# Optimization experiments

Hardware: AMD Instinct MI355X
Metric: run time of the kernel (lower is better)

The kernel has to match this reference:

```python
import jax, jax.numpy as jnp
import numpy as np

# Upper-triangular index pattern used by convert_Avec_to_A (row-major triu of 4x4 -> 10 entries)
_TRIU_R, _TRIU_C = np.triu_indices(4)


def _A_vec_to_A(A_vec):
    """(B,10) -> (B,4,4) symmetric matrix, filling upper triangle row-major then mirroring."""
    B = A_vec.shape[0]
    A = jnp.zeros((B, 4, 4), dtype=A_vec.dtype)
    A = A.at[:, _TRIU_R, _TRIU_C].set(A_vec)
    A = A.at[:, _TRIU_C, _TRIU_R].set(A_vec)
    return A


def setup_inputs() -> dict:
    key = jax.random.key(0)
    k1, k2 = jax.random.split(key)
    B = 1048576
    A_vec_pred = jax.random.normal(k1, (B, 10), dtype=jnp.float32)
    q_target = jax.random.normal(k2, (B, 4), dtype=jnp.float32)
    q_target = q_target / jnp.linalg.norm(q_target, axis=-1, keepdims=True)  # unit quaternions
    return {"A_vec_pred": A_vec_pred, "q_target": q_target}


def reference(A_vec_pred, q_target):
    # A_vec_to_quat(-A_vec_pred): eigenvector of minimum eigenvalue of sym(-A_vec)
    A = _A_vec_to_A(-A_vec_pred)                 # (B,4,4)
    _, evs = jnp.linalg.eigh(A)                  # eigenvalues ascending; columns = eigenvectors
    q_pred = evs[:, :, 0]                        # (B,4) min-eigenvalue eigenvector (unit norm)
    # quat_chordal_squared_loss: d = min(||q-qt||, ||q+qt||); losses = 2*d^2*(4-d^2)
    d2 = jnp.minimum(jnp.sum((q_pred - q_target) ** 2, axis=-1),
                     jnp.sum((q_pred + q_target) ** 2, axis=-1))
    losses = 2.0 * d2 * (4.0 - d2)
    return losses.mean()
```

## Files before the change

### kernel.cpp

```cpp
#include <hip/hip_runtime.h>


#define TPB 256
#define PAIRS 2

typedef float vf4 __attribute__((ext_vector_type(4)));

struct Pair { vf4 f0, f1, f2, f3, f4, q0, q1; };

__device__ __forceinline__ void issue_loads(const float* a, const float* q,
                                            Pair& d) {
    unsigned long long aa = (unsigned long long)a;
    unsigned long long qq = (unsigned long long)q;
    asm volatile("global_load_dwordx4 %0, %1, off"           : "=v"(d.f0) : "v"(aa));
    asm volatile("global_load_dwordx4 %0, %1, off offset:16" : "=v"(d.f1) : "v"(aa));
    asm volatile("global_load_dwordx4 %0, %1, off offset:32" : "=v"(d.f2) : "v"(aa));
    asm volatile("global_load_dwordx4 %0, %1, off offset:48" : "=v"(d.f3) : "v"(aa));
    asm volatile("global_load_dwordx4 %0, %1, off offset:64" : "=v"(d.f4) : "v"(aa));
    asm volatile("global_load_dwordx4 %0, %1, off"           : "=v"(d.q0) : "v"(qq));
    asm volatile("global_load_dwordx4 %0, %1, off offset:16" : "=v"(d.q1) : "v"(qq));
}

__device__ __forceinline__ void cross4(const float* x, const float* y,
                                       const float* z, float* w) {
    float m01 = y[0]*z[1] - y[1]*z[0];
    float m02 = y[0]*z[2] - y[2]*z[0];
    float m03 = y[0]*z[3] - y[3]*z[0];
    float m12 = y[1]*z[2] - y[2]*z[1];
    float m13 = y[1]*z[3] - y[3]*z[1];
    float m23 = y[2]*z[3] - y[3]*z[2];
    w[0] =  (x[1]*m23 - x[2]*m13 + x[3]*m12);
    w[1] = -(x[0]*m23 - x[2]*m03 + x[3]*m02);
    w[2] =  (x[0]*m13 - x[1]*m03 + x[3]*m01);
    w[3] = -(x[0]*m12 - x[1]*m02 + x[2]*m01);
}

__device__ __forceinline__ float det3s(float p, float q, float r,
                                       float s, float t, float u) {
    return p*(s*u - t*t) - q*(q*u - r*t) + r*(q*t - r*s);
}

__device__ __forceinline__ float solve_elem(const float a[10], float4 qt) {
    float m00 = -a[0], m01 = -a[1], m02 = -a[2], m03 = -a[3];
    float m11 = -a[4], m12 = -a[5], m13 = -a[6];
    float m22 = -a[7], m23 = -a[8], m33 = -a[9];

    float e1 = m00 + m11 + m22 + m33;
    float e2 = m00*m11 - m01*m01 + m00*m22 - m02*m02 + m00*m33 - m03*m03
             + m11*m22 - m12*m12 + m11*m33 - m13*m13 + m22*m33 - m23*m23;
    float e3 = det3s(m11, m12, m13, m22, m23, m33)
             + det3s(m00, m02, m03, m22, m23, m33)
             + det3s(m00, m01, m03, m11, m13, m33)
             + det3s(m00, m01, m02, m11, m12, m22);
    float r1v[4] = {m01, m11, m12, m13};
    float r2v[4] = {m02, m12, m22, m23};
    float r3v[4] = {m03, m13, m23, m33};
    float cw[4];
    cross4(r1v, r2v, r3v, cw);
    float e4 = m00*cw[0] + m01*cw[1] + m02*cw[2] + m03*cw[3];

    float s0 = fabsf(m01) + fabsf(m02) + fabsf(m03);
    float s1 = fabsf(m01) + fabsf(m12) + fabsf(m13);
    float s2 = fabsf(m02) + fabsf(m12) + fabsf(m23);
    float s3 = fabsf(m03) + fabsf(m13) + fabsf(m23);
    float lo = fminf(fminf(m00 - s0, m11 - s1), fminf(m22 - s2, m33 - s3)) - 1e-3f;
    float hi = fminf(fminf(m00, m11), fminf(m22, m33));
    float lam = lo;
    #pragma unroll
    for (int it = 0; it < 8; ++it) {
        float p  = (((lam - e1)*lam + e2)*lam - e3)*lam + e4;
        float dp = ((4.f*lam - 3.f*e1)*lam + 2.f*e2)*lam - e3;
        dp = fminf(dp, -1e-12f);
        lam = lam - p * __builtin_amdgcn_rcpf(dp);
        lam = fminf(fmaxf(lam, lo), hi);
    }

    float R0[4] = {m00 - lam, m01, m02, m03};
    float R1[4] = {m01, m11 - lam, m12, m13};
    float R2[4] = {m02, m12, m22 - lam, m23};
    float R3[4] = {m03, m13, m23, m33 - lam};
    float c0[4], c1[4], c2[4], c3[4];
    cross4(R1, R2, R3, c0);
    cross4(R0, R2, R3, c1);
    cross4(R0, R1, R3, c2);
    cross4(R0, R1, R2, c3);
    float n0 = c0[0]*c0[0] + c0[1]*c0[1] + c0[2]*c0[2] + c0[3]*c0[3];
    float n1 = c1[0]*c1[0] + c1[1]*c1[1] + c1[2]*c1[2] + c1[3]*c1[3];
    float n2 = c2[0]*c2[0] + c2[1]*c2[1] + c2[2]*c2[2] + c2[3]*c2[3];
    float n3 = c3[0]*c3[0] + c3[1]*c3[1] + c3[2]*c3[2] + c3[3]*c3[3];

    float bn = n0, w0 = c0[0], w1 = c0[1], w2 = c0[2], w3 = c0[3];
    bool b;
    b = n1 > bn; bn = b ? n1 : bn; w0 = b ? c1[0] : w0; w1 = b ? c1[1] : w1;
                 w2 = b ? c1[2] : w2; w3 = b ? c1[3] : w3;
    b = n2 > bn; bn = b ? n2 : bn; w0 = b ? c2[0] : w0; w1 = b ? c2[1] : w1;
                 w2 = b ? c2[2] : w2; w3 = b ? c2[3] : w3;
    b = n3 > bn; bn = b ? n3 : bn; w0 = b ? c3[0] : w0; w1 = b ? c3[1] : w1;
                 w2 = b ? c3[2] : w2; w3 = b ? c3[3] : w3;

    float d = w0*qt.x + w1*qt.y + w2*qt.z + w3*qt.w;
    float inv = __builtin_amdgcn_rcpf(fmaxf(bn, 1e-20f));
    float loss = 8.f * (bn - d*d) * inv;
    return fminf(fmaxf(loss, 0.f), 8.f);
}

template <int CTRL, int ROW_MASK>
__device__ __forceinline__ float dpp_add(float v) {
    int t = __builtin_amdgcn_update_dpp(0, __builtin_bit_cast(int, v),
                                        CTRL, ROW_MASK, 0xf, true);
    return v + __builtin_bit_cast(float, t);
}

__device__ __forceinline__ float wave_sum(float v) {
    v = dpp_add<0x111, 0xf>(v);
    v = dpp_add<0x112, 0xf>(v);
    v = dpp_add<0x114, 0xf>(v);
    v = dpp_add<0x118, 0xf>(v);
    v = dpp_add<0x142, 0xa>(v);
    v = dpp_add<0x143, 0xc>(v);
    return __builtin_bit_cast(float,
        __builtin_amdgcn_readlane(__builtin_bit_cast(int, v), 63));
}

__global__ __launch_bounds__(TPB) void qcqp_loss_kernel(
    const float* __restrict__ A_vec, const float* __restrict__ q_t,
    float* __restrict__ part, int B, int T)
{
    int t = blockIdx.x * blockDim.x + threadIdx.x;
    int Ptot = B >> 1;
    float lsum = 0.f;

    Pair Pd, Nd;
    int curp = t;
    {
        int c = (curp < Ptot) ? curp : 0;
        issue_loads(A_vec + (size_t)c * 20, q_t + (size_t)c * 8, Pd);
    }
    int nxtp = curp;

    #define STEP(K, VMSTR)                                                    \
    {                                                                         \
        if ((K) + 1 < PAIRS) {                                                \
            nxtp = t + ((K) + 1) * T;                                         \
            int nc = (nxtp < Ptot) ? nxtp : 0;                                \
            issue_loads(A_vec + (size_t)nc * 20, q_t + (size_t)nc * 8, Nd);   \
        }                                                                     \
        asm volatile("s_waitcnt vmcnt(" VMSTR ")" ::: "memory");              \
        __builtin_amdgcn_sched_barrier(0);                                    \
        {                                                                     \
            bool ok = (curp < Ptot);                                          \
            float a0[10] = {Pd.f0.x, Pd.f0.y, Pd.f0.z, Pd.f0.w,               \
                            Pd.f1.x, Pd.f1.y, Pd.f1.z, Pd.f1.w,               \
                            Pd.f2.x, Pd.f2.y};                                \
            float a1[10] = {Pd.f2.z, Pd.f2.w, Pd.f3.x, Pd.f3.y,               \
                            Pd.f3.z, Pd.f3.w, Pd.f4.x, Pd.f4.y,               \
                            Pd.f4.z, Pd.f4.w};                                \
            float4 qt0 = make_float4(Pd.q0.x, Pd.q0.y, Pd.q0.z, Pd.q0.w);     \
            float4 qt1 = make_float4(Pd.q1.x, Pd.q1.y, Pd.q1.z, Pd.q1.w);     \
            float L0 = solve_elem(a0, qt0);                                   \
            float L1 = solve_elem(a1, qt1);                                   \
            lsum += ok ? (L0 + L1) : 0.f;                                     \
        }                                                                     \
        Pd = Nd; curp = nxtp;                                                 \
    }

    STEP(0, "7")
    STEP(1, "0")
    #undef STEP

    float wsum = wave_sum(lsum);

    __shared__ float sm[TPB / 64];
    int lane = threadIdx.x & 63, wid = threadIdx.x >> 6;
    if (lane == 0) sm[wid] = wsum;
    __syncthreads();
    if (threadIdx.x == 0)
        part[blockIdx.x] = sm[0] + sm[1] + sm[2] + sm[3];
}

__global__ __launch_bounds__(TPB) void qcqp_reduce_kernel(
    const float* __restrict__ part, const float* __restrict__ A_vec,
    const float* __restrict__ q_t, float* __restrict__ out,
    int nparts, int B)
{
    float s = 0.f;
    for (int i = threadIdx.x; i < nparts; i += TPB)
        s += part[i];
    float wsum = wave_sum(s);

    __shared__ float sm[TPB / 64];
    int lane = threadIdx.x & 63, wid = threadIdx.x >> 6;
    if (lane == 0) sm[wid] = wsum;
    __syncthreads();
    if (threadIdx.x == 0) {
        float total = sm[0] + sm[1] + sm[2] + sm[3];
        if (B & 1) {
            const float* av = A_vec + (size_t)(B - 1) * 10;
            float2 v01 = *(const float2*)(av + 0);
            float2 v23 = *(const float2*)(av + 2);
            float2 v45 = *(const float2*)(av + 4);
            float2 v67 = *(const float2*)(av + 6);
            float2 v89 = *(const float2*)(av + 8);
            float a0[10] = {v01.x, v01.y, v23.x, v23.y, v45.x,
                            v45.y, v67.x, v67.y, v89.x, v89.y};
            float4 qt0 = *(const float4*)(q_t + (size_t)(B - 1) * 4);
            total += solve_elem(a0, qt0);
        }
        out[0] = total / (float)B;
    }
}

extern "C" void kernel_launch(void* const* d_in, const int* in_sizes, int n_in,
                              void* d_out, int out_size, void* d_ws, size_t ws_size,
                              hipStream_t stream)
{
    const float* A_vec = (const float*)d_in[0];
    const float* q_t   = (const float*)d_in[1];
    int B = in_sizes[0] / 10;
    float* part = (float*)d_ws;

    int Ptot = B >> 1;
    int nblocks = (Ptot + TPB * PAIRS - 1) / (TPB * PAIRS);
    int T = nblocks * TPB;
    qcqp_loss_kernel<<<nblocks, TPB, 0, stream>>>(A_vec, q_t, part, B, T);
    qcqp_reduce_kernel<<<1, TPB, 0, stream>>>(part, A_vec, q_t,
                                              (float*)d_out, nblocks, B);
}
```

Measured before the change: 19.81 us.

## Pack two eigen-solves into float2 vectors and use one combined cofactor eigenvector

Each thread now solves its two 4x4 problems together in float2 vectors, so the compiler can emit packed FP32 instructions (v_pk_fma/v_pk_mul) that do two lanes per instruction. The eigenvector step no longer computes four cofactor cross products and picks the largest. It builds a single vector from shared 2x2 minors and combinations of rows. The 3x3 minors feeding e3 and e4 are also shared. Together these cut VALU work in a compute-bound kernel. The risk is lower robustness when the single combined vector is near-degenerate, and extra register pressure or swizzle moves from the packing.

```diff
diff --git a/kernel.cpp b/kernel.cpp
--- a/kernel.cpp
+++ b/kernel.cpp
@@ -5,6 +5,7 @@
 #define PAIRS 2
 
 typedef float vf4 __attribute__((ext_vector_type(4)));
+typedef float vf2 __attribute__((ext_vector_type(2)));
 
 struct Pair { vf4 f0, f1, f2, f3, f4, q0, q1; };
 
@@ -21,87 +22,103 @@
     asm volatile("global_load_dwordx4 %0, %1, off offset:16" : "=v"(d.q1) : "v"(qq));
 }
 
-__device__ __forceinline__ void cross4(const float* x, const float* y,
-                                       const float* z, float* w) {
-    float m01 = y[0]*z[1] - y[1]*z[0];
-    float m02 = y[0]*z[2] - y[2]*z[0];
-    float m03 = y[0]*z[3] - y[3]*z[0];
-    float m12 = y[1]*z[2] - y[2]*z[1];
-    float m13 = y[1]*z[3] - y[3]*z[1];
-    float m23 = y[2]*z[3] - y[3]*z[2];
-    w[0] =  (x[1]*m23 - x[2]*m13 + x[3]*m12);
-    w[1] = -(x[0]*m23 - x[2]*m03 + x[3]*m02);
-    w[2] =  (x[0]*m13 - x[1]*m03 + x[3]*m01);
-    w[3] = -(x[0]*m12 - x[1]*m02 + x[2]*m01);
+__device__ __forceinline__ vf2 vmin2(vf2 a, vf2 b){ return __builtin_elementwise_min(a,b); }
+__device__ __forceinline__ vf2 vmax2(vf2 a, vf2 b){ return __builtin_elementwise_max(a,b); }
+__device__ __forceinline__ vf2 vabs2(vf2 a){ return __builtin_elementwise_abs(a); }
+__device__ __forceinline__ vf2 splat2(float s){ vf2 r; r.x = s; r.y = s; return r; }
+__device__ __forceinline__ vf2 rcp2(vf2 a){
+    vf2 r; r.x = __builtin_amdgcn_rcpf(a.x); r.y = __builtin_amdgcn_rcpf(a.y);
+    return r;
+}
+
+__device__ __forceinline__ vf2 solve_pair(const vf2 a[10],
+                                          vf2 qx, vf2 qy, vf2 qz, vf2 qw) {
+    vf2 m00 = -a[0], m01 = -a[1], m02 = -a[2], m03 = -a[3];
+    vf2 m11 = -a[4], m12 = -a[5], m13 = -a[6];
+    vf2 m22 = -a[7], m23 = -a[8], m33 = -a[9];
+
+    vf2 e1 = m00 + m11 + m22 + m33;
+    vf2 e2 = m00*m11 - m01*m01 + m00*m22 - m02*m02 + m00*m33 - m03*m03
+           + m11*m22 - m12*m12 + m11*m33 - m13*m13 + m22*m33 - m23*m23;
+
+    vf2 x01 = m02*m13 - m12*m03;
+    vf2 x02 = m02*m23 - m22*m03;
+    vf2 x03 = m02*m33 - m23*m03;
+    vf2 x12 = m12*m23 - m22*m13;
+    vf2 x13 = m12*m33 - m23*m13;
+    vf2 x23 = m22*m33 - m23*m23;
+    vf2 cw0 =  (m11*x23 - m12*x13 + m13*x12);
+    vf2 cw1 = -(m01*x23 - m12*x03 + m13*x02);
+    vf2 cw2 =  (m01*x13 - m11*x03 + m13*x01);
+    vf2 cw3 = -(m01*x12 - m11*x02 + m12*x01);
+    vf2 e4 = m00*cw0 + m01*cw1 + m02*cw2 + m03*cw3;
+
+    vf2 e3 = cw0
+           + (m00*x23 - m02*x03 + m03*x02)
+           + (m00*(m11*m33 - m13*m13) - m01*(m01*m33 - m03*m13)
+              + m03*(m01*m13 - m03*m11))
+           + (m00*(m11*m22 - m12*m12) - m01*(m01*m22 - m02*m12)
+              + m02*(m01*m12 - m02*m11));
+
+    vf2 s0v = vabs2(m01) + vabs2(m02) + vabs2(m03);
+    vf2 s1v = vabs2(m01) + vabs2(m12) + vabs2(m13);
+    vf2 s2v = vabs2(m02) + vabs2(m12) + vabs2(m23);
+    vf2 s3v = vabs2(m03) + vabs2(m13) + vabs2(m23);
+    vf2 lo = vmin2(vmin2(m00 - s0v, m11 - s1v), vmin2(m22 - s2v, m33 - s3v))
+           - splat2(1e-3f);
+    vf2 hi = vmin2(vmin2(m00, m11), vmin2(m22, m33));
+    vf2 lam = lo;
+    vf2 ndpcap = splat2(-1e-12f);
+    #pragma unroll
+    for (int it = 0; it < 8; ++it) {
+        vf2 p  = (((lam - e1)*lam + e2)*lam - e3)*lam + e4;
+        vf2 dp = ((4.f*lam - 3.f*e1)*lam + 2.f*e2)*lam - e3;
+        dp = vmin2(dp, ndpcap);
+        lam = lam - p * rcp2(dp);
+        lam = vmin2(vmax2(lam, lo), hi);
+    }
+
+    vf2 r00 = m00 - lam, r11 = m11 - lam, r22 = m22 - lam, r33 = m33 - lam;
+    vf2 sm01 = m02*m13 - m12*m03;
+    vf2 sm02 = m02*m23 - r22*m03;
+    vf2 sm03 = m02*r33 - m23*m03;
+    vf2 sm12 = m12*m23 - r22*m13;
+    vf2 sm13 = m12*r33 - m23*m13;
+    vf2 sm23 = r22*r33 - m23*m23;
+    vf2 tm01 = r00*r11 - m01*m01;
+    vf2 tm02 = r00*m12 - m02*m01;
+    vf2 tm03 = r00*m13 - m03*m01;
+    vf2 tm12 = m01*m12 - m02*r11;
+    vf2 tm13 = m01*m13 - m03*r11;
+    vf2 tm23 = m02*m13 - m03*m12;
+    vf2 u0 = m01 - r00, u1 = r11 - m01, u2 = m12 - m02, u3 = m13 - m03;
+    vf2 y0 = m03 - m02, y1 = m13 - m12, y2 = m23 - r22, y3 = r33 - m23;
+    vf2 w0 =  (u1*sm23 - u2*sm13 + u3*sm12)
+            + (y1*tm23 - y2*tm13 + y3*tm12);
+    vf2 w1 = -(u0*sm23 - u2*sm03 + u3*sm02)
+            - (y0*tm23 - y2*tm03 + y3*tm02);
+    vf2 w2 =  (u0*sm13 - u1*sm03 + u3*sm01)
+            + (y0*tm13 - y1*tm03 + y3*tm01);
+    vf2 w3 = -(u0*sm12 - u1*sm02 + u2*sm01)
+            - (y0*tm12 - y1*tm02 + y2*tm01);
+    vf2 bn = w0*w0 + w1*w1 + w2*w2 + w3*w3;
+
+    vf2 d = w0*qx + w1*qy + w2*qz + w3*qw;
+    vf2 inv = rcp2(vmax2(bn, splat2(1e-20f)));
+    vf2 loss = 8.f * (bn - d*d) * inv;
+    return vmin2(vmax2(loss, splat2(0.f)), splat2(8.f));
 }
 
 __device__ __forceinline__ float det3s(float p, float q, float r,
                                        float s, float t, float u) {
     return p*(s*u - t*t) - q*(q*u - r*t) + r*(q*t - r*s);
 }
-
 __device__ __forceinline__ float solve_elem(const float a[10], float4 qt) {
-    float m00 = -a[0], m01 = -a[1], m02 = -a[2], m03 = -a[3];
-    float m11 = -a[4], m12 = -a[5], m13 = -a[6];
-    float m22 = -a[7], m23 = -a[8], m33 = -a[9];
-
-    float e1 = m00 + m11 + m22 + m33;
-    float e2 = m00*m11 - m01*m01 + m00*m22 - m02*m02 + m00*m33 - m03*m03
-             + m11*m22 - m12*m12 + m11*m33 - m13*m13 + m22*m33 - m23*m23;
-    float e3 = det3s(m11, m12, m13, m22, m23, m33)
-             + det3s(m00, m02, m03, m22, m23, m33)
-             + det3s(m00, m01, m03, m11, m13, m33)
-             + det3s(m00, m01, m02, m11, m12, m22);
-    float r1v[4] = {m01, m11, m12, m13};
-    float r2v[4] = {m02, m12, m22, m23};
-    float r3v[4] = {m03, m13, m23, m33};
-    float cw[4];
-    cross4(r1v, r2v, r3v, cw);
-    float e4 = m00*cw[0] + m01*cw[1] + m02*cw[2] + m03*cw[3];
-
-    float s0 = fabsf(m01) + fabsf(m02) + fabsf(m03);
-    float s1 = fabsf(m01) + fabsf(m12) + fabsf(m13);
-    float s2 = fabsf(m02) + fabsf(m12) + fabsf(m23);
-    float s3 = fabsf(m03) + fabsf(m13) + fabsf(m23);
-    float lo = fminf(fminf(m00 - s0, m11 - s1), fminf(m22 - s2, m33 - s3)) - 1e-3f;
-    float hi = fminf(fminf(m00, m11), fminf(m22, m33));
-    float lam = lo;
+    vf2 aa[10];
     #pragma unroll
-    for (int it = 0; it < 8; ++it) {
-        float p  = (((lam - e1)*lam + e2)*lam - e3)*lam + e4;
-        float dp = ((4.f*lam - 3.f*e1)*lam + 2.f*e2)*lam - e3;
-        dp = fminf(dp, -1e-12f);
-        lam = lam - p * __builtin_amdgcn_rcpf(dp);
-        lam = fminf(fmaxf(lam, lo), hi);
-    }
-
-    float R0[4] = {m00 - lam, m01, m02, m03};
-    float R1[4] = {m01, m11 - lam, m12, m13};
-    float R2[4] = {m02, m12, m22 - lam, m23};
-    float R3[4] = {m03, m13, m23, m33 - lam};
-    float c0[4], c1[4], c2[4], c3[4];
-    cross4(R1, R2, R3, c0);
-    cross4(R0, R2, R3, c1);
-    cross4(R0, R1, R3, c2);
-    cross4(R0, R1, R2, c3);
-    float n0 = c0[0]*c0[0] + c0[1]*c0[1] + c0[2]*c0[2] + c0[3]*c0[3];
-    float n1 = c1[0]*c1[0] + c1[1]*c1[1] + c1[2]*c1[2] + c1[3]*c1[3];
-    float n2 = c2[0]*c2[0] + c2[1]*c2[1] + c2[2]*c2[2] + c2[3]*c2[3];
-    float n3 = c3[0]*c3[0] + c3[1]*c3[1] + c3[2]*c3[2] + c3[3]*c3[3];
-
-    float bn = n0, w0 = c0[0], w1 = c0[1], w2 = c0[2], w3 = c0[3];
-    bool b;
-    b = n1 > bn; bn = b ? n1 : bn; w0 = b ? c1[0] : w0; w1 = b ? c1[1] : w1;
-                 w2 = b ? c1[2] : w2; w3 = b ? c1[3] : w3;
-    b = n2 > bn; bn = b ? n2 : bn; w0 = b ? c2[0] : w0; w1 = b ? c2[1] : w1;
-                 w2 = b ? c2[2] : w2; w3 = b ? c2[3] : w3;
-    b = n3 > bn; bn = b ? n3 : bn; w0 = b ? c3[0] : w0; w1 = b ? c3[1] : w1;
-                 w2 = b ? c3[2] : w2; w3 = b ? c3[3] : w3;
-
-    float d = w0*qt.x + w1*qt.y + w2*qt.z + w3*qt.w;
-    float inv = __builtin_amdgcn_rcpf(fmaxf(bn, 1e-20f));
-    float loss = 8.f * (bn - d*d) * inv;
-    return fminf(fmaxf(loss, 0.f), 8.f);
+    for (int i = 0; i < 10; ++i) { aa[i].x = a[i]; aa[i].y = a[i]; }
+    vf2 L = solve_pair(aa, splat2(qt.x), splat2(qt.y), splat2(qt.z), splat2(qt.w));
+    return L.x;
 }
 
 template <int CTRL, int ROW_MASK>
@@ -149,17 +166,23 @@
         __builtin_amdgcn_sched_barrier(0);                                    \
         {                                                                     \
             bool ok = (curp < Ptot);                                          \
-            float a0[10] = {Pd.f0.x, Pd.f0.y, Pd.f0.z, Pd.f0.w,               \
-                            Pd.f1.x, Pd.f1.y, Pd.f1.z, Pd.f1.w,               \
-                            Pd.f2.x, Pd.f2.y};                                \
-            float a1[10] = {Pd.f2.z, Pd.f2.w, Pd.f3.x, Pd.f3.y,               \
-                            Pd.f3.z, Pd.f3.w, Pd.f4.x, Pd.f4.y,               \
-                            Pd.f4.z, Pd.f4.w};                                \
-            float4 qt0 = make_float4(Pd.q0.x, Pd.q0.y, Pd.q0.z, Pd.q0.w);     \
-            float4 qt1 = make_float4(Pd.q1.x, Pd.q1.y, Pd.q1.z, Pd.q1.w);     \
-            float L0 = solve_elem(a0, qt0);                                   \
-            float L1 = solve_elem(a1, qt1);                                   \
-            lsum += ok ? (L0 + L1) : 0.f;                                     \
+            vf2 aa[10];                                                       \
+            aa[0] = (vf2){Pd.f0.x, Pd.f2.z};                                  \
+            aa[1] = (vf2){Pd.f0.y, Pd.f2.w};                                  \
+            aa[2] = (vf2){Pd.f0.z, Pd.f3.x};                                  \
+            aa[3] = (vf2){Pd.f0.w, Pd.f3.y};                                  \
+            aa[4] = (vf2){Pd.f1.x, Pd.f3.z};                                  \
+            aa[5] = (vf2){Pd.f1.y, Pd.f3.w};                                  \
+            aa[6] = (vf2){Pd.f1.z, Pd.f4.x};                                  \
+            aa[7] = (vf2){Pd.f1.w, Pd.f4.y};                                  \
+            aa[8] = (vf2){Pd.f2.x, Pd.f4.z};                                  \
+            aa[9] = (vf2){Pd.f2.y, Pd.f4.w};                                  \
+            vf2 qx = (vf2){Pd.q0.x, Pd.q1.x};                                 \
+            vf2 qy = (vf2){Pd.q0.y, Pd.q1.y};                                 \
+            vf2 qz = (vf2){Pd.q0.z, Pd.q1.z};                                 \
+            vf2 qw = (vf2){Pd.q0.w, Pd.q1.w};                                 \
+            vf2 L = solve_pair(aa, qx, qy, qz, qw);                           \
+            lsum += ok ? (L.x + L.y) : 0.f;                                   \
         }                                                                     \
         Pd = Nd; curp = nxtp;                                                 \
     }
```

Result: faster. 18.55 us (-6.3%).
